# Kernel optimization log

Measured on AMD Instinct MI355X. Metric: run time of the kernel, lower is better.

The kernel has to match this reference:

```python
import jax, jax.numpy as jnp
import numpy as np

H = 0.01      # RK4 step size (parameter.h)
LAM = 1.0     # stage-cost gate penalty
R_COST = 0.1  # scalar control cost R
WMIN, WMAX = -0.01, 0.01  # disturbance range
B, N_STATES, T_STEPS = 8192, 2, 2048

# substituted plant dynamics (parameter.x1_dot / parameter.x2_dot)
def _x1_dot(x1, x2, u):
    return -2.0 * x1 + x2 + u

def _x2_dot(x1, x2, u):
    return x1 - 2.0 * x2 + u

def _rk4_step(x, u):
    # Faithful to RungeKutta.f: k2 == k3 (both evaluated at x2 + h/2)
    x1, x2 = x[0], x[1]
    k1 = jnp.stack([_x1_dot(x1, x2, u), _x2_dot(x1, x2, u)])
    k2 = jnp.stack([_x1_dot(x1, x2 + H / 2, u), _x2_dot(x1, x2 + H / 2, u)])
    k4 = jnp.stack([_x1_dot(x1, x2 + H, u), _x2_dot(x1, x2 + H, u)])
    return x + H * (k1 + 4.0 * k2 + k4) / 6.0  # (k1+2k2+2k3+k4)/6 with k3=k2


def setup_inputs() -> dict:
    key = jax.random.key(0)
    kw, kK, kL, kM, kMo = jax.random.split(key, 5)
    w = jax.random.uniform(kw, (B, N_STATES, T_STEPS), dtype=jnp.float32,
                           minval=WMIN, maxval=WMAX)
    K = 0.1 * jax.random.normal(kK, (1, N_STATES), dtype=jnp.float32)
    L = 0.05 * jax.random.normal(kL, (2 * N_STATES, 2 * N_STATES), dtype=jnp.float32)
    M = 0.05 * jax.random.normal(kM, (1, 2 * N_STATES), dtype=jnp.float32)
    Mo = 0.05 * jax.random.normal(kMo, (1, 1), dtype=jnp.float32)
    return {"w": w, "K": K, "L": L, "M": M, "Mo": Mo}


def reference(w, K, L, M, Mo):
    # w: (B, N, T) disturbances; returns per-sample trajectory cost J, shape (B,)
    Bsz, N, T = w.shape
    dt = w.dtype
    Q = jnp.eye(N, dtype=dt)
    Qf = 10.0 * jnp.eye(N, dtype=dt)
    x0 = jnp.zeros((N,), dtype=dt).at[0].set(1.0)  # xf = 0
    steps = jnp.arange(T)

    def traj_cost(w_b):  # w_b: (N, T)
        def step(carry, inp):
            x, x_hat = carry          # each (N,)
            w_t, i = inp
            z = jnp.concatenate([x, x_hat])            # phi input (2N,)
            phi = z @ L @ z + M[0] @ z + Mo[0, 0]
            delta = jnp.where(i == 0, jnp.asarray(1.0, dt), jax.nn.sigmoid(phi))
            x_hat_n = jnp.where(i == 0, x_hat, delta * x + (1.0 - delta) * x_hat)
            u = K[0] @ x_hat_n                         # control from gated estimate
            x_next = _rk4_step(x, u) + w_t
            u_s = K[0] @ x                             # J uses K @ x[:,i]
            sc = x @ Q @ x + R_COST * u_s * u_s + LAM * delta
            return (x_next, x_hat_n), sc

        (x_T, _), scs = jax.lax.scan(step, (x0, x0), (w_b.T, steps))
        return jnp.sum(scs[: T - 1]) + x_T @ Qf @ x_T

    return jax.vmap(traj_cost)(w)
```

## Files before the change

### kernel.cpp

```cpp
#include <hip/hip_runtime.h>


#define T_STEPS 2048
#define BATCH   8192

typedef float v2f __attribute__((ext_vector_type(2)));

__device__ __forceinline__ v2f mk2(float a, float b) { v2f r; r.x = a; r.y = b; return r; }

__global__ __launch_bounds__(64, 1) void cstr_kernel(
    const float* __restrict__ w,
    const float* __restrict__ K,
    const float* __restrict__ L,
    const float* __restrict__ M,
    const float* __restrict__ Mo,
    float* __restrict__ out)
{
    const int s = blockIdx.x * 64 + (int)threadIdx.x;

    constexpr float Hs = 0.01f;
    constexpr float Ad = 1.0f - 2.0f * Hs;
    constexpr float Rc = 0.1f;
    constexpr float SC = -1.44269504088896340736f;

    const float k1 = K[0], k2 = K[1];

    const float s11 = L[0] * SC;
    const float s12 = (L[1] + L[4]) * SC;
    const float s13 = (L[2] + L[8]) * SC;
    const float s14 = (L[3] + L[12]) * SC;
    const float s22 = L[5] * SC;
    const float s23 = (L[6] + L[9]) * SC;
    const float s24 = (L[7] + L[13]) * SC;
    const float s33 = L[10] * SC;
    const float s34 = (L[11] + L[14]) * SC;
    const float s44 = L[15] * SC;

    const v2f S11_22 = mk2(s11, s22);
    const v2f S12_0  = mk2(s12, 0.0f);
    const v2f S13_23 = mk2(s13, s23);
    const v2f S14_24 = mk2(s14, s24);
    const v2f S33_44 = mk2(s33, s44);
    const v2f S34_0  = mk2(s34, 0.0f);
    const v2f M12    = mk2(M[0] * SC, M[1] * SC);
    const v2f M34    = mk2(M[2] * SC, M[3] * SC);
    const float kc   = __builtin_amdgcn_exp2f(Mo[0] * SC);

    const v2f HK  = mk2(Hs * k1, Hs * k2);
    const v2f C12 = mk2(0.5f * Hs * Hs, -Hs * Hs);

    v2f x  = mk2(1.0f, 0.0f);
    v2f xh = x;
    v2f acc2  = mk2(0.0f, 0.0f);
    float accXY = 0.0f;
    float accD  = 0.0f;

    auto step = [&](float w1, float w2, bool first, bool cost) {
        v2f   dx  = x - xh;
        v2f   tk  = HK * dx;
        float kdx = tk.x + tk.y;
        v2f   th  = HK * xh;
        float kxh = th.x + th.y;
        v2f   wc  = mk2(w1, w2) + C12;
        v2f   pre = Ad * x + (Hs * mk2(x.y, x.x) + wc);
        v2f   pf  = pre + kxh;

        float d;
        if (first) {
            d = 1.0f;
        } else {
            v2f a   = S11_22 * x + M12;
            a       = S12_0 * x.y + a;
            v2f b   = S13_23 * xh.x;
            b       = S14_24 * xh.y + b;
            v2f g12 = a + b;
            v2f c   = S33_44 * xh + M34;
            v2f g34 = S34_0 * xh.y + c;
            v2f Q   = xh * g34 + x * g12;
            float ph = Q.x + Q.y;
            float E  = __builtin_amdgcn_exp2f(ph);
            d = __builtin_amdgcn_rcpf(fmaf(kc, E, 1.0f));
        }
        if (cost) {
            acc2  = x * x + acc2;
            accXY = fmaf(x.x, x.y, accXY);
            accD += d;
        }
        xh = d * dx + xh;
        x  = d * kdx + pf;
    };

    auto chunk = [&](const float4* b0, const float4* b1, bool first, bool lastc) {
        #pragma unroll
        for (int q = 0; q < 4; ++q) {
            float4 a = b0[q];
            float4 b = b1[q];
            step(a.x, b.x, first && (q == 0), true);
            step(a.y, b.y, false, true);
            step(a.z, b.z, false, true);
            step(a.w, b.w, false, !(lastc && (q == 3)));
        }
    };

    const float4* r0 = reinterpret_cast<const float4*>(w + (size_t)s * 2 * T_STEPS);
    const float4* r1 = reinterpret_cast<const float4*>(w + (size_t)s * 2 * T_STEPS + T_STEPS);

    float4 A0[4], A1[4], B0[4], B1[4];
    #pragma unroll
    for (int q = 0; q < 4; ++q) { A0[q] = r0[q];     A1[q] = r1[q]; }
    #pragma unroll
    for (int q = 0; q < 4; ++q) { B0[q] = r0[4 + q]; B1[q] = r1[4 + q]; }

    chunk(A0, A1, true, false);

    for (int i = 0; i < 63; ++i) {
        const float4* p0 = r0 + (size_t)(2 + 2 * i) * 4;
        const float4* p1 = r1 + (size_t)(2 + 2 * i) * 4;
        #pragma unroll
        for (int q = 0; q < 4; ++q) { A0[q] = p0[q]; A1[q] = p1[q]; }
        chunk(B0, B1, false, false);
        const float4* q0 = r0 + (size_t)(3 + 2 * i) * 4;
        const float4* q1 = r1 + (size_t)(3 + 2 * i) * 4;
        #pragma unroll
        for (int q = 0; q < 4; ++q) { B0[q] = q0[q]; B1[q] = q1[q]; }
        chunk(A0, A1, false, false);
    }
    chunk(B0, B1, false, true);

    float sum_us2 = fmaf(k1 * k1, acc2.x,
                    fmaf(k2 * k2, acc2.y, 2.0f * k1 * k2 * accXY));
    acc2 = 10.0f * (x * x) + acc2;
    float J = acc2.x + acc2.y + Rc * sum_us2 + accD;
    out[s] = J;
}

extern "C" void kernel_launch(void* const* d_in, const int* in_sizes, int n_in,
                              void* d_out, int out_size, void* d_ws, size_t ws_size,
                              hipStream_t stream) {
    const float* w  = (const float*)d_in[0];
    const float* K  = (const float*)d_in[1];
    const float* L  = (const float*)d_in[2];
    const float* M  = (const float*)d_in[3];
    const float* Mo = (const float*)d_in[4];
    float* out = (float*)d_out;

    hipLaunchKernelGGL(cstr_kernel, dim3(BATCH / 64), dim3(64), 0, stream,
                       w, K, L, M, Mo, out);
}
```

Before: 313.2 us.

## Restructure recurrence to precompute phi, hand-code packed FMA asm, halve chunk size

The gate logit phi for the next step is now computed at the end of each step from the updated state, so the exp/rcp for the gate starts a step ahead and the dependency chain is rearranged. The first-step special case is handled by starting phi at -inf, which makes the gate equal 1. The arithmetic is written as inline v_pk_fma/v_pk_mul/v_pk_add asm with op_sel to avoid swizzle moves, and the per-chunk prefetch buffer shrinks from 16 to 8 steps. Inline asm hides these instructions from the compiler's scheduler, and the smaller buffer leaves less prefetch distance to cover memory latency.

Result: no change. 312.7 us (-0.1%).

```diff
diff --git a/kernel.cpp b/kernel.cpp
--- a/kernel.cpp
+++ b/kernel.cpp
@@ -7,6 +7,46 @@
 typedef float v2f __attribute__((ext_vector_type(2)));
 
 __device__ __forceinline__ v2f mk2(float a, float b) { v2f r; r.x = a; r.y = b; return r; }
+
+__device__ __forceinline__ v2f pk_fma(v2f a, v2f b, v2f c) {
+    v2f d;
+    asm("v_pk_fma_f32 %0, %1, %2, %3" : "=v"(d) : "v"(a), "v"(b), "v"(c));
+    return d;
+}
+__device__ __forceinline__ v2f pk_fma_b1lo(v2f a, v2f b, v2f c) {
+    v2f d;
+    asm("v_pk_fma_f32 %0, %1, %2, %3 op_sel:[0,0,0] op_sel_hi:[1,0,1]"
+        : "=v"(d) : "v"(a), "v"(b), "v"(c));
+    return d;
+}
+__device__ __forceinline__ v2f pk_fma_b1hi(v2f a, v2f b, v2f c) {
+    v2f d;
+    asm("v_pk_fma_f32 %0, %1, %2, %3 op_sel:[0,1,0] op_sel_hi:[1,1,1]"
+        : "=v"(d) : "v"(a), "v"(b), "v"(c));
+    return d;
+}
+__device__ __forceinline__ v2f pk_fma_b1swap(v2f a, v2f b, v2f c) {
+    v2f d;
+    asm("v_pk_fma_f32 %0, %1, %2, %3 op_sel:[0,1,0] op_sel_hi:[1,0,1]"
+        : "=v"(d) : "v"(a), "v"(b), "v"(c));
+    return d;
+}
+__device__ __forceinline__ v2f pk_mul(v2f a, v2f b) {
+    v2f d;
+    asm("v_pk_mul_f32 %0, %1, %2" : "=v"(d) : "v"(a), "v"(b));
+    return d;
+}
+__device__ __forceinline__ v2f pk_add(v2f a, v2f b) {
+    v2f d;
+    asm("v_pk_add_f32 %0, %1, %2" : "=v"(d) : "v"(a), "v"(b));
+    return d;
+}
+__device__ __forceinline__ v2f pk_hadd(v2f a) {
+    v2f d;
+    asm("v_pk_add_f32 %0, %1, %2 op_sel:[0,1] op_sel_hi:[1,0]"
+        : "=v"(d) : "v"(a), "v"(a));
+    return d;
+}
 
 __global__ __launch_bounds__(64, 1) void cstr_kernel(
     const float* __restrict__ w,
@@ -25,112 +65,110 @@
 
     const float k1 = K[0], k2 = K[1];
 
-    const float s11 = L[0] * SC;
-    const float s12 = (L[1] + L[4]) * SC;
-    const float s13 = (L[2] + L[8]) * SC;
-    const float s14 = (L[3] + L[12]) * SC;
-    const float s22 = L[5] * SC;
-    const float s23 = (L[6] + L[9]) * SC;
-    const float s24 = (L[7] + L[13]) * SC;
-    const float s33 = L[10] * SC;
-    const float s34 = (L[11] + L[14]) * SC;
-    const float s44 = L[15] * SC;
+    const float u11 = L[0] * SC;
+    const float u12 = (L[1] + L[4]) * SC;
+    const float u13 = (L[2] + L[8]) * SC;
+    const float u14 = (L[3] + L[12]) * SC;
+    const float u22 = L[5] * SC;
+    const float u23 = (L[6] + L[9]) * SC;
+    const float u24 = (L[7] + L[13]) * SC;
+    const float u33 = L[10] * SC;
+    const float u34 = (L[11] + L[14]) * SC;
+    const float u44 = L[15] * SC;
 
-    const v2f S11_22 = mk2(s11, s22);
-    const v2f S12_0  = mk2(s12, 0.0f);
-    const v2f S13_23 = mk2(s13, s23);
-    const v2f S14_24 = mk2(s14, s24);
-    const v2f S33_44 = mk2(s33, s44);
-    const v2f S34_0  = mk2(s34, 0.0f);
-    const v2f M12    = mk2(M[0] * SC, M[1] * SC);
-    const v2f M34    = mk2(M[2] * SC, M[3] * SC);
-    const float kc   = __builtin_amdgcn_exp2f(Mo[0] * SC);
+    const v2f Ua  = mk2(u11, u22);
+    const v2f Ub  = mk2(u12, 0.0f);
+    const v2f Uc  = mk2(u13, u23);
+    const v2f Ud  = mk2(u14, u24);
+    const v2f Ue  = mk2(u33, u44);
+    const v2f Uf  = mk2(u34, 0.0f);
+    const v2f M12 = mk2(M[0] * SC, M[1] * SC);
+    const v2f M34 = mk2(M[2] * SC, M[3] * SC);
+    const float kc = __builtin_amdgcn_exp2f(Mo[0] * SC);
 
-    const v2f HK  = mk2(Hs * k1, Hs * k2);
-    const v2f C12 = mk2(0.5f * Hs * Hs, -Hs * Hs);
+    const v2f AD2  = mk2(Ad, Ad);
+    const v2f HS2  = mk2(Hs, Hs);
+    const v2f HK2  = mk2(Hs * k1, Hs * k2);
+    const v2f NEG1 = mk2(-1.0f, -1.0f);
+    const float C1v = 0.5f * Hs * Hs;
+    const float C2v = -Hs * Hs;
 
-    v2f x  = mk2(1.0f, 0.0f);
-    v2f xh = x;
-    v2f acc2  = mk2(0.0f, 0.0f);
-    float accXY = 0.0f;
-    float accD  = 0.0f;
+    v2f X  = mk2(1.0f, 0.0f);
+    v2f Hh = X;
+    v2f accA = mk2(0.0f, 0.0f);
+    float aXY = 0.0f;
+    float aD  = 0.0f;
+    float phi = __int_as_float(0xff800000u);
 
-    auto step = [&](float w1, float w2, bool first, bool cost) {
-        v2f   dx  = x - xh;
-        v2f   tk  = HK * dx;
-        float kdx = tk.x + tk.y;
-        v2f   th  = HK * xh;
-        float kxh = th.x + th.y;
-        v2f   wc  = mk2(w1, w2) + C12;
-        v2f   pre = Ad * x + (Hs * mk2(x.y, x.x) + wc);
-        v2f   pf  = pre + kxh;
-
-        float d;
-        if (first) {
-            d = 1.0f;
-        } else {
-            v2f a   = S11_22 * x + M12;
-            a       = S12_0 * x.y + a;
-            v2f b   = S13_23 * xh.x;
-            b       = S14_24 * xh.y + b;
-            v2f g12 = a + b;
-            v2f c   = S33_44 * xh + M34;
-            v2f g34 = S34_0 * xh.y + c;
-            v2f Q   = xh * g34 + x * g12;
-            float ph = Q.x + Q.y;
-            float E  = __builtin_amdgcn_exp2f(ph);
-            d = __builtin_amdgcn_rcpf(fmaf(kc, E, 1.0f));
+    auto step = [&](float w1, float w2, bool cost) {
+        float E = __builtin_amdgcn_exp2f(phi);
+        float y = fmaf(kc, E, 1.0f);
+        float d = __builtin_amdgcn_rcpf(y);
+        v2f dX = pk_fma(Hh, NEG1, X);
+        v2f Hn; Hn.x = fmaf(d, dX.x, Hh.x); Hn.y = fmaf(d, dX.y, Hh.y);
+        v2f P2  = pk_mul(HK2, Hn);
+        v2f HU2 = pk_hadd(P2);
+        v2f Wc; Wc.x = w1 + C1v; Wc.y = w2 + C2v;
+        v2f Bv  = pk_add(Wc, HU2);
+        v2f Xin = pk_fma_b1swap(HS2, X, Bv);
+        v2f Xn  = pk_fma(AD2, X, Xin);
+        if (cost) {
+            accA = pk_fma(X, X, accA);
+            aXY  = fmaf(X.x, X.y, aXY);
+            aD  += d;
         }
-        if (cost) {
-            acc2  = x * x + acc2;
-            accXY = fmaf(x.x, x.y, accXY);
-            accD += d;
-        }
-        xh = d * dx + xh;
-        x  = d * kdx + pf;
+        X = Xn; Hh = Hn;
+        v2f T12 = pk_fma(Ua, X, M12);
+        T12 = pk_fma_b1hi(Ub, X, T12);
+        T12 = pk_fma_b1lo(Uc, Hh, T12);
+        T12 = pk_fma_b1hi(Ud, Hh, T12);
+        v2f T34 = pk_fma(Ue, Hh, M34);
+        T34 = pk_fma_b1hi(Uf, Hh, T34);
+        v2f Pp = pk_mul(X, T12);
+        Pp = pk_fma(Hh, T34, Pp);
+        phi = Pp.x + Pp.y;
     };
 
-    auto chunk = [&](const float4* b0, const float4* b1, bool first, bool lastc) {
+    auto chunk = [&](const float4* b0, const float4* b1, bool lastc) {
         #pragma unroll
-        for (int q = 0; q < 4; ++q) {
+        for (int q = 0; q < 2; ++q) {
             float4 a = b0[q];
             float4 b = b1[q];
-            step(a.x, b.x, first && (q == 0), true);
-            step(a.y, b.y, false, true);
-            step(a.z, b.z, false, true);
-            step(a.w, b.w, false, !(lastc && (q == 3)));
+            step(a.x, b.x, true);
+            step(a.y, b.y, true);
+            step(a.z, b.z, true);
+            step(a.w, b.w, !(lastc && (q == 1)));
         }
     };
 
     const float4* r0 = reinterpret_cast<const float4*>(w + (size_t)s * 2 * T_STEPS);
     const float4* r1 = reinterpret_cast<const float4*>(w + (size_t)s * 2 * T_STEPS + T_STEPS);
 
-    float4 A0[4], A1[4], B0[4], B1[4];
+    float4 A0[2], A1[2], B0[2], B1[2];
     #pragma unroll
-    for (int q = 0; q < 4; ++q) { A0[q] = r0[q];     A1[q] = r1[q]; }
+    for (int q = 0; q < 2; ++q) { A0[q] = r0[q];     A1[q] = r1[q]; }
     #pragma unroll
-    for (int q = 0; q < 4; ++q) { B0[q] = r0[4 + q]; B1[q] = r1[4 + q]; }
+    for (int q = 0; q < 2; ++q) { B0[q] = r0[2 + q]; B1[q] = r1[2 + q]; }
 
-    chunk(A0, A1, true, false);
+    chunk(A0, A1, false);
 
-    for (int i = 0; i < 63; ++i) {
-        const float4* p0 = r0 + (size_t)(2 + 2 * i) * 4;
-        const float4* p1 = r1 + (size_t)(2 + 2 * i) * 4;
+    for (int i = 0; i < 127; ++i) {
+        const float4* p0 = r0 + (size_t)(2 + 2 * i) * 2;
+        const float4* p1 = r1 + (size_t)(2 + 2 * i) * 2;
         #pragma unroll
-        for (int q = 0; q < 4; ++q) { A0[q] = p0[q]; A1[q] = p1[q]; }
-        chunk(B0, B1, false, false);
-        const float4* q0 = r0 + (size_t)(3 + 2 * i) * 4;
-        const float4* q1 = r1 + (size_t)(3 + 2 * i) * 4;
+        for (int q = 0; q < 2; ++q) { A0[q] = p0[q]; A1[q] = p1[q]; }
+        chunk(B0, B1, false);
+        const float4* q0 = r0 + (size_t)(3 + 2 * i) * 2;
+        const float4* q1 = r1 + (size_t)(3 + 2 * i) * 2;
         #pragma unroll
-        for (int q = 0; q < 4; ++q) { B0[q] = q0[q]; B1[q] = q1[q]; }
-        chunk(A0, A1, false, false);
+        for (int q = 0; q < 2; ++q) { B0[q] = q0[q]; B1[q] = q1[q]; }
+        chunk(A0, A1, false);
     }
-    chunk(B0, B1, false, true);
+    chunk(B0, B1, true);
 
-    float sum_us2 = fmaf(k1 * k1, acc2.x,
-                    fmaf(k2 * k2, acc2.y, 2.0f * k1 * k2 * accXY));
-    acc2 = 10.0f * (x * x) + acc2;
-    float J = acc2.x + acc2.y + Rc * sum_us2 + accD;
+    float us2 = fmaf(k1 * k1, accA.x, fmaf(k2 * k2, accA.y, 2.0f * k1 * k2 * aXY));
+    float J = accA.x + accA.y + Rc * us2 + aD
+            + 10.0f * fmaf(X.x, X.x, X.y * X.y);
     out[s] = J;
 }
 
```
